# Kernel tuning notes

Measured on AMD Instinct MI355X. Metric: run time of the kernel, lower is better.

Reference implementation:

```python
import jax, jax.numpy as jnp
import numpy as np

DIM, B, H, W = 96, 2, 64, 64
D_INNER, D_STATE, DT_RANK, K = 2 * DIM, 16, 6, 4


def _conv2d(x, w, b=None, padding=0, dilation=1, groups=1):
    out = jax.lax.conv_general_dilated(
        x, w, (1, 1), [(padding, padding)] * 2,
        rhs_dilation=(dilation, dilation),
        dimension_numbers=('NCHW', 'OIHW', 'NCHW'),
        feature_group_count=groups)
    return out if b is None else out + b[None, :, None, None]


def _layernorm(x, g, b, eps=1e-5):
    mu = x.mean(-1, keepdims=True)
    xc = x - mu
    var = (xc * xc).mean(-1, keepdims=True)
    return xc * jax.lax.rsqrt(var + eps) * g + b


def _chan_recal(t, w1, w2):
    s = t.mean((2, 3)) + t.max(axis=(2, 3))          # GAP + GMP, (B,C)
    w = jax.nn.sigmoid(jax.nn.relu(s @ w1.T) @ w2.T)
    return t * w[:, :, None, None]


def _selective_scan(u, delta, A, Bm, Cm, D):
    # u, delta: (B,K,d,L); A: (K,d,N); Bm,Cm: (B,K,N,L); D: (K,d)
    Bsz, Kk, d, L = u.shape
    N = A.shape[-1]
    seq = (jnp.moveaxis(delta, -1, 0), jnp.moveaxis(u, -1, 0),
           jnp.moveaxis(Bm, -1, 0), jnp.moveaxis(Cm, -1, 0))
    h0 = jnp.zeros((Bsz, Kk, d, N), u.dtype)

    def step(h, inp):
        dl, ul, bl, cl = inp  # (B,K,d),(B,K,d),(B,K,N),(B,K,N)
        h = jnp.exp(dl[..., None] * A) * h + (dl * ul)[..., None] * bl[:, :, None, :]
        return h, (h * cl[:, :, None, :]).sum(-1)

    _, ys = jax.lax.scan(step, h0, seq)
    return jnp.moveaxis(ys, 0, -1) + D[None, :, :, None] * u  # (B,K,d,L)


def _ss2d(x, in_proj_w, conv_w, conv_b, x_proj_w, dt_w, dt_b,
          A_logs, Ds, out_norm_g, out_norm_b, out_proj_w):
    Bsz, Hh, Ww, C = x.shape
    d = in_proj_w.shape[0] // 2
    xm, z = jnp.split(x @ in_proj_w.T, 2, axis=-1)
    xm = jnp.transpose(xm, (0, 3, 1, 2))  # (B,d,H,W)
    xm = jax.nn.silu(_conv2d(xm, conv_w, conv_b, padding=1, groups=d))
    L = Hh * Ww
    x_hw = xm.reshape(Bsz, d, L)
    x_wh = jnp.transpose(xm, (0, 1, 3, 2)).reshape(Bsz, d, L)
    xs = jnp.stack([x_hw, x_wh, x_hw[..., ::-1], x_wh[..., ::-1]], axis=1)  # (B,4,d,L)
    x_dbl = jnp.einsum('bkdl,kcd->bkcl', xs, x_proj_w)
    r = dt_w.shape[-1]
    N = A_logs.shape[-1]
    dts, Bs, Cs = jnp.split(x_dbl, [r, r + N], axis=2)
    dts = jax.nn.softplus(jnp.einsum('bkrl,kdr->bkdl', dts, dt_w) + dt_b[None, :, :, None])
    out_y = _selective_scan(xs, dts, -jnp.exp(A_logs), Bs, Cs, Ds)
    inv_y = out_y[:, 2:4, :, ::-1]
    wh = lambda t: jnp.transpose(t.reshape(Bsz, d, Ww, Hh), (0, 1, 3, 2)).reshape(Bsz, d, L)
    y = out_y[:, 0] + inv_y[:, 0] + wh(out_y[:, 1]) + wh(inv_y[:, 1])
    y = _layernorm(jnp.transpose(y, (0, 2, 1)).reshape(Bsz, Hh, Ww, d), out_norm_g, out_norm_b)
    return (y * jax.nn.silu(z)) @ out_proj_w.T


def _forward(x, arf_w1, arf_b1, arf_w2, arf_b2, arf_w3, arf_b3, arf_w4, arf_b4,
             fuse_w, fuse_b, edge_w, enh_w1, enh_b1, bn_g, bn_b, enh_w2, enh_b2,
             pre_fc1, pre_fc2, norm_g, norm_b, in_proj_w, ss_conv_w, ss_conv_b,
             x_proj_w, dt_w, dt_b, A_logs, Ds, out_norm_g, out_norm_b, out_proj_w,
             post_fc1, post_fc2, proj_w, proj_b):
    shortcut = x
    C = x.shape[1]
    g = C // 4
    # AdaptiveReceptiveField (fc gating branch is dead code in the original forward)
    f1 = _conv2d(x, arf_w1, arf_b1, padding=1, dilation=1, groups=g)
    f2 = _conv2d(x, arf_w2, arf_b2, padding=2, dilation=2, groups=g)
    f3 = _conv2d(x, arf_w3, arf_b3, padding=4, dilation=4, groups=g)
    f4 = _conv2d(x, arf_w4, arf_b4, padding=8, dilation=8, groups=g)
    h = _conv2d(jnp.concatenate([f1, f2, f3, f4], 1), fuse_w, fuse_b)
    # LearnableEdgeEnhancement (BatchNorm in training mode: batch stats, biased var)
    edge = _conv2d(h, edge_w, None, padding=1, groups=C)
    e = _conv2d(edge, enh_w1, enh_b1)
    mu = e.mean((0, 2, 3), keepdims=True)
    var = ((e - mu) ** 2).mean((0, 2, 3), keepdims=True)
    e = jax.nn.relu((e - mu) * jax.lax.rsqrt(var + 1e-5) * bn_g[None, :, None, None]
                    + bn_b[None, :, None, None])
    h = h * (1.0 + jax.nn.sigmoid(_conv2d(e, enh_w2, enh_b2)))
    h = _chan_recal(h, pre_fc1, pre_fc2)
    hn = _layernorm(jnp.transpose(h, (0, 2, 3, 1)), norm_g, norm_b)
    hn = _ss2d(hn, in_proj_w, ss_conv_w, ss_conv_b, x_proj_w, dt_w, dt_b,
               A_logs, Ds, out_norm_g, out_norm_b, out_proj_w)
    h = jnp.transpose(hn, (0, 3, 1, 2))
    h = _chan_recal(h, post_fc1, post_fc2)
    h = _conv2d(h, proj_w, proj_b)
    return shortcut + h


def setup_inputs():
    key = jax.random.key(0)
    ks = iter(jax.random.split(key, 48))
    rn = lambda shape, s=0.05: jax.random.normal(next(ks), shape, jnp.float32) * s
    lap = jnp.array([[0., 1., 0.], [1., -4., 1.], [0., 1., 0.]], jnp.float32)
    q = DIM // 4
    inp = {
        'x': jax.random.normal(next(ks), (B, DIM, H, W), jnp.float32),
        'arf_w1': rn((q, 4, 3, 3)), 'arf_b1': rn((q,)),
        'arf_w2': rn((q, 4, 3, 3)), 'arf_b2': rn((q,)),
        'arf_w3': rn((q, 4, 3, 3)), 'arf_b3': rn((q,)),
        'arf_w4': rn((q, 4, 3, 3)), 'arf_b4': rn((q,)),
        'fuse_w': rn((DIM, DIM, 1, 1)), 'fuse_b': rn((DIM,)),
        'edge_w': jnp.tile(lap[None, None], (DIM, 1, 1, 1)),
        'enh_w1': rn((q, DIM, 1, 1)), 'enh_b1': rn((q,)),
        'bn_g': jnp.ones((q,), jnp.float32), 'bn_b': jnp.zeros((q,), jnp.float32),
        'enh_w2': rn((DIM, q, 1, 1)), 'enh_b2': rn((DIM,)),
        'pre_fc1': rn((q, DIM)), 'pre_fc2': rn((DIM, q)),
        'norm_g': jnp.ones((DIM,), jnp.float32), 'norm_b': jnp.zeros((DIM,), jnp.float32),
        'in_proj_w': rn((2 * D_INNER, DIM)),
        'ss_conv_w': rn((D_INNER, 1, 3, 3)), 'ss_conv_b': rn((D_INNER,)),
        'x_proj_w': rn((K, DT_RANK + 2 * D_STATE, D_INNER)),
        'dt_w': rn((K, D_INNER, DT_RANK), 0.1), 'dt_b': rn((K, D_INNER), 0.1),
        'A_logs': jnp.broadcast_to(jnp.log(jnp.arange(1, D_STATE + 1, dtype=jnp.float32)),
                                   (K, D_INNER, D_STATE)) + jnp.zeros((K, D_INNER, D_STATE), jnp.float32),
        'Ds': jnp.ones((K, D_INNER), jnp.float32),
        'out_norm_g': jnp.ones((D_INNER,), jnp.float32),
        'out_norm_b': jnp.zeros((D_INNER,), jnp.float32),
        'out_proj_w': rn((DIM, D_INNER)),
        'post_fc1': rn((q, DIM)), 'post_fc2': rn((DIM, q)),
        'proj_w': rn((DIM, DIM, 1, 1)), 'proj_b': rn((DIM,)),
    }
    return inp


def reference(x, arf_w1, arf_b1, arf_w2, arf_b2, arf_w3, arf_b3, arf_w4, arf_b4,
              fuse_w, fuse_b, edge_w, enh_w1, enh_b1, bn_g, bn_b, enh_w2, enh_b2,
              pre_fc1, pre_fc2, norm_g, norm_b, in_proj_w, ss_conv_w, ss_conv_b,
              x_proj_w, dt_w, dt_b, A_logs, Ds, out_norm_g, out_norm_b, out_proj_w,
              post_fc1, post_fc2, proj_w, proj_b):
    return _forward(x, arf_w1, arf_b1, arf_w2, arf_b2, arf_w3, arf_b3, arf_w4, arf_b4,
                    fuse_w, fuse_b, edge_w, enh_w1, enh_b1, bn_g, bn_b, enh_w2, enh_b2,
                    pre_fc1, pre_fc2, norm_g, norm_b, in_proj_w, ss_conv_w, ss_conv_b,
                    x_proj_w, dt_w, dt_b, A_logs, Ds, out_norm_g, out_norm_b, out_proj_w,
                    post_fc1, post_fc2, proj_w, proj_b)
```

## Files before the change

### kernel.cpp

```cpp
#include <hip/hip_runtime.h>
#include <cmath>

#define LL   4096
#define HWD  64
#define CCH  96
#define QQ   24
#define DDI  192
#define NST  16
#define NCH  128
#define CLEN 32
#define TSC  32
#define XT2  32
#define XP   108
#define FP   100
#define VP   204

static const size_t OFF_F    = 0;
static const size_t OFF_H    = 786432;
static const size_t OFF_E    = 1572864;
static const size_t OFF_E1PS = 1769472;
static const size_t OFF_E1P2 = 1770240;
static const size_t OFF_XM   = 2556736;
static const size_t OFF_Z    = 4129600;
static const size_t OFF_XC   = 5702464;
static const size_t OFF_DTS  = 7275328;
static const size_t OFF_BC   = 13566784;
static const size_t OFF_YK   = 14615360;
static const size_t OFF_Y2   = 22528832;
static const size_t OFF_HL   = 23315264;
static const size_t OFF_SD   = 26460992;
static const size_t OFF_HIN  = 26657600;
static const size_t OFF_S1PS = 29803328;
static const size_t OFF_S1PM = 29806400;
static const size_t OFF_S2PS = 29809472;
static const size_t OFF_S2PM = 29821760;

static __device__ __forceinline__ int map_k(int k, int l) {
  int ll = (k & 2) ? (LL - 1 - l) : l;
  return (k & 1) ? (((ll & 63) << 6) | (ll >> 6)) : ll;
}

__global__ __launch_bounds__(256) void k_arf(const float* __restrict__ x,
    const float* __restrict__ w1, const float* __restrict__ b1,
    const float* __restrict__ w2, const float* __restrict__ b2,
    const float* __restrict__ w3, const float* __restrict__ b3,
    const float* __restrict__ w4, const float* __restrict__ b4,
    float* __restrict__ f) {
  int idx = blockIdx.x * 256 + threadIdx.x;
  int p = idx & (LL - 1);
  int oc = __builtin_amdgcn_readfirstlane((idx >> 12) % CCH);
  int b  = __builtin_amdgcn_readfirstlane(idx / (CCH * LL));
  int i = oc / QQ, q = oc % QQ;
  int dil = 1 << i;
  const float* w  = (i == 0 ? w1 : i == 1 ? w2 : i == 2 ? w3 : w4) + q * 36;
  const float* bb = (i == 0 ? b1 : i == 1 ? b2 : i == 2 ? b3 : b4);
  int yy0 = p >> 6, xx0 = p & 63;
  float acc = bb[q];
  const float* xin = x + ((size_t)b * CCH + q * 4) * LL;
  #pragma unroll
  for (int ky = 0; ky < 3; ky++) {
    int yy = yy0 + (ky - 1) * dil;
    if (yy < 0 || yy >= HWD) continue;
    #pragma unroll
    for (int kx = 0; kx < 3; kx++) {
      int xx = xx0 + (kx - 1) * dil;
      if (xx < 0 || xx >= HWD) continue;
      int pp = (yy << 6) + xx;
      #pragma unroll
      for (int ci = 0; ci < 4; ci++)
        acc += w[ci * 9 + ky * 3 + kx] * xin[(size_t)ci * LL + pp];
    }
  }
  f[idx] = acc;
}

__global__ __launch_bounds__(256) void k_fuse(const float* __restrict__ f,
    const float* __restrict__ fw, const float* __restrict__ fb, float* __restrict__ h) {
  int pix0 = blockIdx.x * 64;
  int oc0 = blockIdx.y * 48;
  int b = pix0 >> 12, p0 = pix0 & (LL - 1);
  int t = threadIdx.x;
  __shared__ float fs[64][FP];
  __shared__ float wbuf[48 * 96];
  for (int i = t; i < 96 * 16; i += 256) {
    int c = i >> 4, q = i & 15;
    float4 v = *(const float4*)(f + ((size_t)b * CCH + c) * LL + p0 + q * 4);
    fs[q * 4 + 0][c] = v.x; fs[q * 4 + 1][c] = v.y;
    fs[q * 4 + 2][c] = v.z; fs[q * 4 + 3][c] = v.w;
  }
  {
    const float4* src = (const float4*)(fw + (size_t)oc0 * CCH);
    float4* dst = (float4*)wbuf;
    for (int i = t; i < 48 * 24; i += 256) dst[i] = src[i];
  }
  __syncthreads();
  int px = t & 63;
  int cg2 = __builtin_amdgcn_readfirstlane(t >> 6);
  float acc[12];
  #pragma unroll
  for (int j = 0; j < 12; j++) acc[j] = 0.f;
  for (int c4 = 0; c4 < 24; c4++) {
    float4 xv = *(const float4*)(&fs[px][c4 * 4]);
    #pragma unroll
    for (int j = 0; j < 12; j++) {
      float4 wv = *(const float4*)(&wbuf[(cg2 * 12 + j) * 96 + c4 * 4]);
      acc[j] = fmaf(xv.x, wv.x, fmaf(xv.y, wv.y, fmaf(xv.z, wv.z, fmaf(xv.w, wv.w, acc[j]))));
    }
  }
  __syncthreads();
  float* ot = &fs[0][0];
  #pragma unroll
  for (int j = 0; j < 12; j++) ot[px * 49 + cg2 * 12 + j] = acc[j];
  __syncthreads();
  for (int i = t; i < 48 * 64; i += 256) {
    int o = i >> 6, p2 = i & 63;
    h[((size_t)b * CCH + oc0 + o) * LL + p0 + p2] = ot[p2 * 49 + o] + fb[oc0 + o];
  }
}

__global__ __launch_bounds__(256) void k_edge(const float* __restrict__ h,
    const float* __restrict__ ew, float* __restrict__ edge) {
  int idx = blockIdx.x * 256 + threadIdx.x;
  int p = idx & (LL - 1);
  int c = __builtin_amdgcn_readfirstlane((idx >> 12) % CCH);
  int b = __builtin_amdgcn_readfirstlane(idx / (CCH * LL));
  int yy0 = p >> 6, xx0 = p & 63;
  const float* w = ew + c * 9;
  const float* hr = h + ((size_t)b * CCH + c) * LL;
  float acc = 0.f;
  #pragma unroll
  for (int ky = 0; ky < 3; ky++) {
    int yy = yy0 + ky - 1;
    if (yy < 0 || yy >= HWD) continue;
    #pragma unroll
    for (int kx = 0; kx < 3; kx++) {
      int xx = xx0 + kx - 1;
      if (xx < 0 || xx >= HWD) continue;
      acc += w[ky * 3 + kx] * hr[(yy << 6) + xx];
    }
  }
  edge[idx] = acc;
}

__global__ __launch_bounds__(256) void k_e1(const float* __restrict__ edge,
    const float* __restrict__ w, const float* __restrict__ bias, float* __restrict__ e,
    float* __restrict__ e1ps, float* __restrict__ e1p2) {
  int tid = threadIdx.x;
  int idx = blockIdx.x * 256 + tid;
  int p = idx & (LL - 1);
  int q = __builtin_amdgcn_readfirstlane((idx >> 12) % QQ);
  int b = __builtin_amdgcn_readfirstlane(idx / (QQ * LL));
  const float* er = edge + (size_t)b * CCH * LL + p;
  const float* wr = w + q * CCH;
  float acc = bias[q];
  for (int c = 0; c < CCH; c++) acc += wr[c] * er[(size_t)c * LL];
  e[idx] = acc;
  __shared__ float rs[256], r2[256];
  rs[tid] = acc; r2[tid] = acc * acc; __syncthreads();
  for (int st = 128; st > 0; st >>= 1) {
    if (tid < st) { rs[tid] += rs[tid + st]; r2[tid] += r2[tid + st]; }
    __syncthreads();
  }
  if (tid == 0) { e1ps[blockIdx.x] = rs[0]; e1p2[blockIdx.x] = r2[0]; }
}

__global__ __launch_bounds__(256) void k_enh(const float* __restrict__ e,
    const float* __restrict__ e1ps, const float* __restrict__ e1p2,
    const float* __restrict__ bn_g, const float* __restrict__ bn_b,
    const float* __restrict__ w2, const float* __restrict__ b2,
    float* __restrict__ h, float* __restrict__ s1ps, float* __restrict__ s1pm) {
  int tid = threadIdx.x;
  __shared__ float bns[QQ], bnsh[QQ];
  if (tid < QQ) {
    float s = 0.f, s2 = 0.f;
    #pragma unroll
    for (int b2 = 0; b2 < 2; b2++)
      for (int i = 0; i < 16; i++) {
        int pi = (b2 * QQ + tid) * 16 + i;
        s += e1ps[pi]; s2 += e1p2[pi];
      }
    float mu = s / (2.f * LL);
    float var = s2 / (2.f * LL) - mu * mu;
    float sc = bn_g[tid] * rsqrtf(var + 1e-5f);
    bns[tid] = sc;
    bnsh[tid] = bn_b[tid] - mu * sc;
  }
  __syncthreads();
  int idx = blockIdx.x * 256 + tid;
  int p = idx & (LL - 1);
  int o = __builtin_amdgcn_readfirstlane((idx >> 12) % CCH);
  int b = __builtin_amdgcn_readfirstlane(idx / (CCH * LL));
  const float* er = e + (size_t)b * QQ * LL + p;
  const float* wr = w2 + o * QQ;
  float acc = b2[o];
  #pragma unroll
  for (int q = 0; q < QQ; q++) {
    float en = fmaxf(er[(size_t)q * LL] * bns[q] + bnsh[q], 0.f);
    acc += wr[q] * en;
  }
  float sig = 1.f / (1.f + __expf(-acc));
  float val = h[idx] * (1.f + sig);
  h[idx] = val;
  __shared__ float rsum[256], rmax[256];
  rsum[tid] = val; rmax[tid] = val; __syncthreads();
  for (int st = 128; st > 0; st >>= 1) {
    if (tid < st) { rsum[tid] += rsum[tid + st]; rmax[tid] = fmaxf(rmax[tid], rmax[tid + st]); }
    __syncthreads();
  }
  if (tid == 0) {
    int row = blockIdx.x >> 4, blk = blockIdx.x & 15;
    s1ps[row * 16 + blk] = rsum[0];
    s1pm[row * 16 + blk] = rmax[0];
  }
}

__global__ __launch_bounds__(256) void k_inproj(const float* __restrict__ h,
    const float* __restrict__ s1ps, const float* __restrict__ s1pm,
    const float* __restrict__ fc1, const float* __restrict__ fc2,
    const float* __restrict__ ng, const float* __restrict__ nb,
    const float* __restrict__ W, float* __restrict__ xm, float* __restrict__ z) {
  int pix0 = blockIdx.x * 64;
  int oc0 = blockIdx.y * CCH;
  int b = pix0 >> 12, p0 = pix0 & (LL - 1);
  int t = threadIdx.x;
  __shared__ float xs[64][XP];
  __shared__ float wbuf[CCH * CCH];
  __shared__ float wsm[CCH];
  __shared__ float hid[QQ];
  __shared__ float ps[64][4], ps2[64][4];
  __shared__ float mu_s[64], rs_s[64];
  if (t < CCH) {
    const float4* sp = (const float4*)(s1ps + (size_t)(b * CCH + t) * 16);
    const float4* mp = (const float4*)(s1pm + (size_t)(b * CCH + t) * 16);
    float s = 0.f, m = -3.402823466e38f;
    #pragma unroll
    for (int i = 0; i < 4; i++) {
      float4 a = sp[i]; s += a.x + a.y + a.z + a.w;
      float4 c = mp[i]; m = fmaxf(m, fmaxf(fmaxf(c.x, c.y), fmaxf(c.z, c.w)));
    }
    wsm[t] = s / (float)LL + m;
  }
  __syncthreads();
  if (t < QQ) {
    float a = 0.f;
    for (int c = 0; c < CCH; c++) a += wsm[c] * fc1[t * CCH + c];
    hid[t] = fmaxf(a, 0.f);
  }
  __syncthreads();
  float w1v = 0.f;
  if (t < CCH) {
    float a = 0.f;
    #pragma unroll
    for (int q = 0; q < QQ; q++) a += hid[q] * fc2[t * QQ + q];
    w1v = 1.f / (1.f + __expf(-a));
  }
  __syncthreads();
  if (t < CCH) wsm[t] = w1v;
  {
    const float4* src = (const float4*)(W + (size_t)oc0 * CCH);
    float4* dst = (float4*)wbuf;
    for (int i = t; i < CCH * 24; i += 256) dst[i] = src[i];
  }
  __syncthreads();
  for (int i = t; i < CCH * 16; i += 256) {
    int c = i >> 4, q = i & 15;
    float w = wsm[c];
    float4 v = *(const float4*)(h + ((size_t)b * CCH + c) * LL + p0 + q * 4);
    xs[q * 4 + 0][c] = v.x * w; xs[q * 4 + 1][c] = v.y * w;
    xs[q * 4 + 2][c] = v.z * w; xs[q * 4 + 3][c] = v.w * w;
  }
  __syncthreads();
  {
    int px = t & 63, qr = t >> 6;
    float s = 0.f, s2 = 0.f;
    #pragma unroll
    for (int j = 0; j < 24; j++) { float v = xs[px][qr * 24 + j]; s += v; s2 += v * v; }
    ps[px][qr] = s; ps2[px][qr] = s2;
  }
  __syncthreads();
  if (t < 64) {
    float ss = ps[t][0] + ps[t][1] + ps[t][2] + ps[t][3];
    float ss2 = ps2[t][0] + ps2[t][1] + ps2[t][2] + ps2[t][3];
    float mu = ss / (float)CCH;
    mu_s[t] = mu;
    rs_s[t] = rsqrtf(ss2 / (float)CCH - mu * mu + 1e-5f);
  }
  __syncthreads();
  for (int i = t; i < 64 * CCH; i += 256) {
    int px = i / CCH, c = i % CCH;
    xs[px][c] = (xs[px][c] - mu_s[px]) * rs_s[px] * ng[c] + nb[c];
  }
  __syncthreads();
  int li = t & 63;
  int cg2 = __builtin_amdgcn_readfirstlane(t >> 6);
  float acc[24];
  #pragma unroll
  for (int j = 0; j < 24; j++) acc[j] = 0.f;
  for (int dq = 0; dq < 24; dq++) {
    float4 xv = *(const float4*)(&xs[li][dq * 4]);
    #pragma unroll
    for (int j = 0; j < 24; j++) {
      float4 wv = *(const float4*)(&wbuf[(cg2 + 4 * j) * CCH + dq * 4]);
      acc[j] = fmaf(xv.x, wv.x, fmaf(xv.y, wv.y, fmaf(xv.z, wv.z, fmaf(xv.w, wv.w, acc[j]))));
    }
  }
  __syncthreads();
  float* ot = &xs[0][0];
  #pragma unroll
  for (int j = 0; j < 24; j++) ot[li * 97 + cg2 + 4 * j] = acc[j];
  __syncthreads();
  float* dst = (oc0 < DDI) ? xm : z;
  int od0 = oc0 % DDI;
  for (int i = t; i < 64 * 96; i += 256) {
    int row = i / 96, c = i % 96;
    dst[(size_t)(pix0 + row) * DDI + od0 + c] = ot[row * 97 + c];
  }
}

__global__ __launch_bounds__(256) void k_ssconv(const float* __restrict__ xm,
    const float* __restrict__ w, const float* __restrict__ bias, float* __restrict__ xc) {
  int idx = blockIdx.x * 256 + threadIdx.x;
  int d = idx % DDI;
  int rem = idx / DDI;
  int xx0 = rem & 63;
  int y0 = ((rem >> 6) & 31) * 2;
  int b = idx / (DDI * LL / 2);
  float wv[9];
  #pragma unroll
  for (int i = 0; i < 9; i++) wv[i] = w[d * 9 + i];
  float acc0 = bias[d], acc1 = bias[d];
  const float* xr = xm + (size_t)b * LL * DDI + d;
  #pragma unroll
  for (int ky = -1; ky <= 2; ky++) {
    int yy = y0 + ky;
    if (yy < 0 || yy >= HWD) continue;
    #pragma unroll
    for (int kx = -1; kx <= 1; kx++) {
      int xx = xx0 + kx;
      if (xx < 0 || xx >= HWD) continue;
      float val = xr[(size_t)((yy << 6) + xx) * DDI];
      if (ky <= 1) acc0 += wv[(ky + 1) * 3 + (kx + 1)] * val;
      if (ky >= 0) acc1 += wv[ky * 3 + (kx + 1)] * val;
    }
  }
  size_t o0 = ((size_t)b * LL + (y0 << 6) + xx0) * DDI + d;
  xc[o0] = acc0 / (1.f + __expf(-acc0));
  xc[o0 + 64 * DDI] = acc1 / (1.f + __expf(-acc1));
}

__global__ __launch_bounds__(256) void k_xdbl(const float* __restrict__ xc,
    const float* __restrict__ xpw, float* __restrict__ dtr_ws, float* __restrict__ bcb) {
  int lt = blockIdx.x;
  int bk = blockIdx.y;
  int b = bk >> 2, k = bk & 3;
  int t = threadIdx.x;
  __shared__ float xs[XT2][XP];
  __shared__ float wbuf[38 * 96];
  int l0 = lt * XT2;
  int pos = t & 31;
  int cg2 = t >> 5;
  float acc[5];
  #pragma unroll
  for (int j = 0; j < 5; j++) acc[j] = 0.f;
  for (int h = 0; h < 2; h++) {
    __syncthreads();
    for (int i = t; i < XT2 * 24; i += 256) {
      int row = i / 24, dq = i % 24;
      int p = map_k(k, l0 + row);
      *(float4*)(&xs[row][dq * 4]) =
          *(const float4*)(xc + ((size_t)b * LL + p) * DDI + h * 96 + dq * 4);
    }
    for (int i = t; i < 38 * 24; i += 256) {
      int c = i / 24, dq = i % 24;
      *(float4*)(&wbuf[c * 96 + dq * 4]) =
          *(const float4*)(xpw + ((size_t)k * 38 + c) * DDI + h * 96 + dq * 4);
    }
    __syncthreads();
    for (int dq = 0; dq < 24; dq++) {
      float4 xv = *(const float4*)(&xs[pos][dq * 4]);
      #pragma unroll
      for (int j = 0; j < 5; j++) {
        int c = cg2 + 8 * j;
        if (c < 38) {
          float4 wv = *(const float4*)(&wbuf[c * 96 + dq * 4]);
          acc[j] = fmaf(xv.x, wv.x, fmaf(xv.y, wv.y, fmaf(xv.z, wv.z, fmaf(xv.w, wv.w, acc[j]))));
        }
      }
    }
  }
  #pragma unroll
  for (int j = 0; j < 5; j++) {
    int c = cg2 + 8 * j;
    if (c < 6) dtr_ws[((size_t)bk * LL + l0 + pos) * 6 + c] = acc[j];
    else if (c < 38) bcb[((size_t)bk * LL + l0 + pos) * 32 + (c - 6)] = acc[j];
  }
}

template <int PASS>
__global__ __launch_bounds__(192) void k_scan(const float* __restrict__ dtr_ws,
    const float* __restrict__ bcb, const float* __restrict__ xc,
    const float* __restrict__ A_logs, const float* __restrict__ dtw,
    const float* __restrict__ dtb, float* __restrict__ hl, float* __restrict__ sd,
    const float* __restrict__ hin, float* __restrict__ yk) {
  int ch = blockIdx.x, bk = blockIdx.y;
  int b = bk >> 2, k = bk & 3;
  int d = threadIdx.x;
  __shared__ float u_s[TSC][DDI];
  __shared__ float bcs[TSC][32];
  __shared__ float dtr_s[TSC][6];
  float Av[NST];
  #pragma unroll
  for (int n = 0; n < NST; n++) Av[n] = -__expf(A_logs[(size_t)(k * DDI + d) * NST + n]);
  bool pw = true;
  #pragma unroll
  for (int n = 1; n < NST; n++) pw = pw && (fabsf(Av[n] - (float)(n + 1) * Av[0]) <= 1e-3f * (n + 1));
  float wdt[6];
  #pragma unroll
  for (int r = 0; r < 6; r++) wdt[r] = dtw[((size_t)(k * DDI + d)) * 6 + r];
  float bdt = dtb[k * DDI + d];
  float h[NST];
  if (PASS == 0) {
    #pragma unroll
    for (int n = 0; n < NST; n++) h[n] = 0.f;
  } else {
    const float* hp = hin + ((size_t)(bk * DDI + d) * NCH + ch) * NST;
    #pragma unroll
    for (int n = 0; n < NST; n++) h[n] = hp[n];
  }
  float sumdt = 0.f;
  int l0 = ch * CLEN;
  {
    for (int i = d; i < TSC * (DDI / 4); i += 192) {
      int row = i / (DDI / 4), q = i % (DDI / 4);
      int p = map_k(k, l0 + row);
      ((float4*)u_s)[i] = *(const float4*)(xc + ((size_t)b * LL + p) * DDI + q * 4);
    }
    {
      const float4* src = (const float4*)(bcb + ((size_t)bk * LL + l0) * 32);
      float4* dst = (float4*)bcs;
      for (int i = d; i < TSC * 32 / 4; i += 192) dst[i] = src[i];
    }
    for (int i = d; i < TSC * 6; i += 192)
      ((float*)dtr_s)[i] = dtr_ws[((size_t)bk * LL + l0) * 6 + i];
    __syncthreads();
    for (int tt = 0; tt < TSC; tt++) {
      float a = bdt;
      #pragma unroll
      for (int r = 0; r < 6; r++) a = fmaf(wdt[r], dtr_s[tt][r], a);
      float dt = (a > 15.f) ? a : __logf(1.f + __expf(a));
      float u  = u_s[tt][d];
      float dtu = dt * u;
      if (PASS == 0) sumdt += dt;
      float eA[NST];
      if (pw) {
        float E = __expf(dt * Av[0]);
        float en = 1.f;
        #pragma unroll
        for (int n = 0; n < NST; n++) { en *= E; eA[n] = en; }
      } else {
        #pragma unroll
        for (int n = 0; n < NST; n++) eA[n] = __expf(dt * Av[n]);
      }
      float y = 0.f;
      #pragma unroll
      for (int n = 0; n < NST; n++) {
        h[n] = eA[n] * h[n] + dtu * bcs[tt][n];
        y += h[n] * bcs[tt][16 + n];
      }
      if (PASS == 1) {
        int p = map_k(k, l0 + tt);
        yk[((size_t)bk * LL + p) * DDI + d] = y;
      }
    }
  }
  if (PASS == 0) {
    float* hp = hl + ((size_t)(bk * DDI + d) * NCH + ch) * NST;
    #pragma unroll
    for (int n = 0; n < NST; n++) hp[n] = h[n];
    sd[(size_t)(bk * DDI + d) * NCH + ch] = sumdt;
  }
}

__global__ __launch_bounds__(256) void k_carry(const float* __restrict__ A_logs,
    const float* __restrict__ hl, const float* __restrict__ sd, float* __restrict__ hin) {
  int idx = blockIdx.x * 256 + threadIdx.x;
  int n = idx & 15;
  int d = (idx >> 4) % DDI;
  int bk = idx / (DDI * NST);
  int k = bk & 3;
  float Aval = -__expf(A_logs[(size_t)(k * DDI + d) * NST + n]);
  float h = 0.f;
  size_t base = (size_t)(bk * DDI + d) * NCH;
  for (int ch = 0; ch < NCH; ch++) {
    hin[(base + ch) * NST + n] = h;
    h = __expf(Aval * sd[base + ch]) * h + hl[(base + ch) * NST + n];
  }
}

__global__ __launch_bounds__(256) void k_outproj(const float* __restrict__ yk,
    const float* __restrict__ xc, const float* __restrict__ Ds, const float* __restrict__ z,
    const float* __restrict__ ong, const float* __restrict__ onb,
    const float* __restrict__ W, float* __restrict__ y2,
    float* __restrict__ s2ps, float* __restrict__ s2pm) {
  int pix0 = blockIdx.x * 64;
  int oc0 = blockIdx.y * 48;
  int b = pix0 >> 12, p0 = pix0 & (LL - 1);
  int t = threadIdx.x;
  __shared__ float xs[64][VP];
  __shared__ float wbuf[48 * 96];
  __shared__ float dsum[DDI];
  __shared__ float ps[64][4], ps2[64][4];
  __shared__ float mu_s[64], rs_s[64];
  if (t < 48) {
    float4 a  = *(const float4*)(Ds + t * 4);
    float4 c1 = *(const float4*)(Ds + DDI + t * 4);
    float4 c2 = *(const float4*)(Ds + 2 * DDI + t * 4);
    float4 c3 = *(const float4*)(Ds + 3 * DDI + t * 4);
    *(float4*)(&dsum[t * 4]) = make_float4(a.x + c1.x + c2.x + c3.x, a.y + c1.y + c2.y + c3.y,
                                           a.z + c1.z + c2.z + c3.z, a.w + c1.w + c2.w + c3.w);
  }
  __syncthreads();
  int px = t & 63, qr = t >> 6;
  int p = p0 + px;
  size_t pb = ((size_t)b * LL + p) * DDI;
  size_t yb = ((size_t)b * 4 * LL + p) * DDI;
  {
    float s = 0.f, s2 = 0.f;
    #pragma unroll
    for (int j = 0; j < 12; j++) {
      int c = (qr * 12 + j) * 4;
      float4 y0 = *(const float4*)(yk + yb + c);
      float4 y1 = *(const float4*)(yk + yb + (size_t)LL * DDI + c);
      float4 y2v = *(const float4*)(yk + yb + 2ul * LL * DDI + c);
      float4 y3 = *(const float4*)(yk + yb + 3ul * LL * DDI + c);
      float4 u = *(const float4*)(xc + pb + c);
      float4 dv = *(const float4*)(&dsum[c]);
      float4 v;
      v.x = y0.x + y1.x + y2v.x + y3.x + dv.x * u.x;
      v.y = y0.y + y1.y + y2v.y + y3.y + dv.y * u.y;
      v.z = y0.z + y1.z + y2v.z + y3.z + dv.z * u.z;
      v.w = y0.w + y1.w + y2v.w + y3.w + dv.w * u.w;
      *(float4*)(&xs[px][c]) = v;
      s += v.x + v.y + v.z + v.w;
      s2 += v.x * v.x + v.y * v.y + v.z * v.z + v.w * v.w;
    }
    ps[px][qr] = s; ps2[px][qr] = s2;
  }
  __syncthreads();
  if (t < 64) {
    float ss = ps[t][0] + ps[t][1] + ps[t][2] + ps[t][3];
    float ss2 = ps2[t][0] + ps2[t][1] + ps2[t][2] + ps2[t][3];
    float mu = ss / (float)DDI;
    mu_s[t] = mu;
    rs_s[t] = rsqrtf(ss2 / (float)DDI - mu * mu + 1e-5f);
  }
  __syncthreads();
  {
    float mu = mu_s[px], rs = rs_s[px];
    #pragma unroll
    for (int j = 0; j < 12; j++) {
      int c = (qr * 12 + j) * 4;
      float4 v = *(const float4*)(&xs[px][c]);
      float4 zz = *(const float4*)(z + pb + c);
      float4 og = *(const float4*)(ong + c);
      float4 ob = *(const float4*)(onb + c);
      float4 gv;
      gv.x = ((v.x - mu) * rs * og.x + ob.x) * (zz.x / (1.f + __expf(-zz.x)));
      gv.y = ((v.y - mu) * rs * og.y + ob.y) * (zz.y / (1.f + __expf(-zz.y)));
      gv.z = ((v.z - mu) * rs * og.z + ob.z) * (zz.z / (1.f + __expf(-zz.z)));
      gv.w = ((v.w - mu) * rs * og.w + ob.w) * (zz.w / (1.f + __expf(-zz.w)));
      *(float4*)(&xs[px][c]) = gv;
    }
  }
  int li = px;
  int cg2 = __builtin_amdgcn_readfirstlane(qr);
  float acc[12];
  #pragma unroll
  for (int j = 0; j < 12; j++) acc[j] = 0.f;
  for (int hh = 0; hh < 2; hh++) {
    __syncthreads();
    for (int i = t; i < 48 * 24; i += 256) {
      int c = i / 24, dq = i % 24;
      *(float4*)(&wbuf[c * 96 + dq * 4]) =
          *(const float4*)(W + (size_t)(oc0 + c) * DDI + hh * 96 + dq * 4);
    }
    __syncthreads();
    for (int dq = 0; dq < 24; dq++) {
      float4 xv = *(const float4*)(&xs[li][hh * 96 + dq * 4]);
      #pragma unroll
      for (int j = 0; j < 12; j++) {
        float4 wv = *(const float4*)(&wbuf[(cg2 + 4 * j) * 96 + dq * 4]);
        acc[j] = fmaf(xv.x, wv.x, fmaf(xv.y, wv.y, fmaf(xv.z, wv.z, fmaf(xv.w, wv.w, acc[j]))));
      }
    }
  }
  int lane = t & 63;
  #pragma unroll
  for (int j = 0; j < 12; j++) {
    float sv = acc[j], mv = acc[j];
    #pragma unroll
    for (int o = 32; o > 0; o >>= 1) {
      sv += __shfl_xor(sv, o);
      mv = fmaxf(mv, __shfl_xor(mv, o));
    }
    if (lane == 0) {
      int oc = oc0 + cg2 + 4 * j;
      int tile = blockIdx.x & 63;
      s2ps[(size_t)(b * CCH + oc) * 64 + tile] = sv;
      s2pm[(size_t)(b * CCH + oc) * 64 + tile] = mv;
    }
  }
  __syncthreads();
  float* ot = &xs[0][0];
  #pragma unroll
  for (int j = 0; j < 12; j++) ot[li * 49 + cg2 + 4 * j] = acc[j];
  __syncthreads();
  for (int i = t; i < 48 * 64; i += 256) {
    int o = i / 64, pi = i % 64;
    y2[((size_t)b * CCH + oc0 + o) * LL + p0 + pi] = ot[pi * 49 + o];
  }
}

__global__ __launch_bounds__(256) void k_final(const float* __restrict__ x,
    const float* __restrict__ y2, const float* __restrict__ s2ps, const float* __restrict__ s2pm,
    const float* __restrict__ fc1, const float* __restrict__ fc2,
    const float* __restrict__ pw, const float* __restrict__ pb, float* __restrict__ out) {
  int pix0 = blockIdx.x * 64;
  int oc0 = blockIdx.y * 48;
  int b = pix0 >> 12, p0 = pix0 & (LL - 1);
  int t = threadIdx.x;
  __shared__ float fs[64][FP];
  __shared__ float wbuf[48 * 96];
  __shared__ float wsm[CCH];
  __shared__ float hid[QQ];
  if (t < CCH) {
    const float4* sp = (const float4*)(s2ps + (size_t)(b * CCH + t) * 64);
    const float4* mp = (const float4*)(s2pm + (size_t)(b * CCH + t) * 64);
    float s = 0.f, m = -3.402823466e38f;
    #pragma unroll
    for (int i = 0; i < 16; i++) {
      float4 a = sp[i]; s += a.x + a.y + a.z + a.w;
      float4 c = mp[i]; m = fmaxf(m, fmaxf(fmaxf(c.x, c.y), fmaxf(c.z, c.w)));
    }
    wsm[t] = s / (float)LL + m;
  }
  __syncthreads();
  if (t < QQ) {
    float a = 0.f;
    for (int c = 0; c < CCH; c++) a += wsm[c] * fc1[t * CCH + c];
    hid[t] = fmaxf(a, 0.f);
  }
  __syncthreads();
  float w2v = 0.f;
  if (t < CCH) {
    float a = 0.f;
    #pragma unroll
    for (int q = 0; q < QQ; q++) a += hid[q] * fc2[t * QQ + q];
    w2v = 1.f / (1.f + __expf(-a));
  }
  __syncthreads();
  if (t < CCH) wsm[t] = w2v;
  __syncthreads();
  for (int i = t; i < 96 * 16; i += 256) {
    int c = i >> 4, q = i & 15;
    float4 v = *(const float4*)(y2 + ((size_t)b * CCH + c) * LL + p0 + q * 4);
    fs[q * 4 + 0][c] = v.x; fs[q * 4 + 1][c] = v.y;
    fs[q * 4 + 2][c] = v.z; fs[q * 4 + 3][c] = v.w;
  }
  for (int i = t; i < 48 * 24; i += 256) {
    int row = i / 24, q = i % 24;
    float4 wv = *(const float4*)(pw + (size_t)(oc0 + row) * CCH + q * 4);
    ((float4*)wbuf)[i] = make_float4(wv.x * wsm[q * 4], wv.y * wsm[q * 4 + 1],
                                     wv.z * wsm[q * 4 + 2], wv.w * wsm[q * 4 + 3]);
  }
  __syncthreads();
  int px = t & 63;
  int cg2 = __builtin_amdgcn_readfirstlane(t >> 6);
  float acc[12];
  #pragma unroll
  for (int j = 0; j < 12; j++) acc[j] = 0.f;
  for (int c4 = 0; c4 < 24; c4++) {
    float4 xv = *(const float4*)(&fs[px][c4 * 4]);
    #pragma unroll
    for (int j = 0; j < 12; j++) {
      float4 wv = *(const float4*)(&wbuf[(cg2 * 12 + j) * 96 + c4 * 4]);
      acc[j] = fmaf(xv.x, wv.x, fmaf(xv.y, wv.y, fmaf(xv.z, wv.z, fmaf(xv.w, wv.w, acc[j]))));
    }
  }
  __syncthreads();
  float* ot = &fs[0][0];
  #pragma unroll
  for (int j = 0; j < 12; j++) ot[px * 49 + cg2 * 12 + j] = acc[j];
  __syncthreads();
  for (int i = t; i < 48 * 64; i += 256) {
    int o = i >> 6, p2 = i & 63;
    size_t oi = ((size_t)b * CCH + oc0 + o) * LL + p0 + p2;
    out[oi] = x[oi] + pb[oc0 + o] + ot[p2 * 49 + o];
  }
}

extern "C" void kernel_launch(void* const* d_in, const int* in_sizes, int n_in,
                              void* d_out, int out_size, void* d_ws, size_t ws_size,
                              hipStream_t stream) {
  const float* x        = (const float*)d_in[0];
  const float* arf_w1   = (const float*)d_in[1];
  const float* arf_b1   = (const float*)d_in[2];
  const float* arf_w2   = (const float*)d_in[3];
  const float* arf_b2   = (const float*)d_in[4];
  const float* arf_w3   = (const float*)d_in[5];
  const float* arf_b3   = (const float*)d_in[6];
  const float* arf_w4   = (const float*)d_in[7];
  const float* arf_b4   = (const float*)d_in[8];
  const float* fuse_w   = (const float*)d_in[9];
  const float* fuse_b   = (const float*)d_in[10];
  const float* edge_w   = (const float*)d_in[11];
  const float* enh_w1   = (const float*)d_in[12];
  const float* enh_b1   = (const float*)d_in[13];
  const float* bn_g     = (const float*)d_in[14];
  const float* bn_b     = (const float*)d_in[15];
  const float* enh_w2   = (const float*)d_in[16];
  const float* enh_b2   = (const float*)d_in[17];
  const float* pre_fc1  = (const float*)d_in[18];
  const float* pre_fc2  = (const float*)d_in[19];
  const float* norm_g   = (const float*)d_in[20];
  const float* norm_b   = (const float*)d_in[21];
  const float* in_proj_w= (const float*)d_in[22];
  const float* ss_conv_w= (const float*)d_in[23];
  const float* ss_conv_b= (const float*)d_in[24];
  const float* x_proj_w = (const float*)d_in[25];
  const float* dt_w     = (const float*)d_in[26];
  const float* dt_b     = (const float*)d_in[27];
  const float* A_logs   = (const float*)d_in[28];
  const float* Ds       = (const float*)d_in[29];
  const float* out_ng   = (const float*)d_in[30];
  const float* out_nb   = (const float*)d_in[31];
  const float* out_proj_w = (const float*)d_in[32];
  const float* post_fc1 = (const float*)d_in[33];
  const float* post_fc2 = (const float*)d_in[34];
  const float* proj_w   = (const float*)d_in[35];
  const float* proj_b   = (const float*)d_in[36];

  float* ws = (float*)d_ws;
  float* fbuf  = ws + OFF_F;
  float* hbuf  = ws + OFF_H;
  float* ebuf  = ws + OFF_E;
  float* e1ps  = ws + OFF_E1PS;
  float* e1p2  = ws + OFF_E1P2;
  float* xmbuf = ws + OFF_XM;
  float* zbuf  = ws + OFF_Z;
  float* xcbuf = ws + OFF_XC;
  float* dtrbuf= ws + OFF_DTS;
  float* bcbuf = ws + OFF_BC;
  float* ykbuf = ws + OFF_YK;
  float* y2buf = ws + OFF_Y2;
  float* hlbuf = ws + OFF_HL;
  float* sdbuf = ws + OFF_SD;
  float* hinbuf= ws + OFF_HIN;
  float* s1ps  = ws + OFF_S1PS;
  float* s1pm  = ws + OFF_S1PM;
  float* s2ps  = ws + OFF_S2PS;
  float* s2pm  = ws + OFF_S2PM;

  k_arf<<<3072, 256, 0, stream>>>(x, arf_w1, arf_b1, arf_w2, arf_b2, arf_w3, arf_b3, arf_w4, arf_b4, fbuf);
  k_fuse<<<dim3(128, 2), 256, 0, stream>>>(fbuf, fuse_w, fuse_b, hbuf);
  k_edge<<<3072, 256, 0, stream>>>(hbuf, edge_w, fbuf);
  k_e1<<<768, 256, 0, stream>>>(fbuf, enh_w1, enh_b1, ebuf, e1ps, e1p2);
  k_enh<<<3072, 256, 0, stream>>>(ebuf, e1ps, e1p2, bn_g, bn_b, enh_w2, enh_b2, hbuf, s1ps, s1pm);
  k_inproj<<<dim3(128, 4), 256, 0, stream>>>(hbuf, s1ps, s1pm, pre_fc1, pre_fc2, norm_g, norm_b, in_proj_w, xmbuf, zbuf);
  k_ssconv<<<3072, 256, 0, stream>>>(xmbuf, ss_conv_w, ss_conv_b, xcbuf);
  k_xdbl<<<dim3(LL / XT2, 8), 256, 0, stream>>>(xcbuf, x_proj_w, dtrbuf, bcbuf);
  k_scan<0><<<dim3(NCH, 8), 192, 0, stream>>>(dtrbuf, bcbuf, xcbuf, A_logs, dt_w, dt_b, hlbuf, sdbuf, nullptr, nullptr);
  k_carry<<<96, 256, 0, stream>>>(A_logs, hlbuf, sdbuf, hinbuf);
  k_scan<1><<<dim3(NCH, 8), 192, 0, stream>>>(dtrbuf, bcbuf, xcbuf, A_logs, dt_w, dt_b, nullptr, nullptr, hinbuf, ykbuf);
  k_outproj<<<dim3(128, 2), 256, 0, stream>>>(ykbuf, xcbuf, Ds, zbuf, out_ng, out_nb, out_proj_w, y2buf, s2ps, s2pm);
  k_final<<<dim3(128, 2), 256, 0, stream>>>(x, y2buf, s2ps, s2pm, post_fc1, post_fc2, proj_w, proj_b, (float*)d_out);
  (void)in_sizes; (void)n_in; (void)out_size; (void)ws_size;
}
```

Baseline: 221.6 us.

## Fuse edge conv with enh 1x1 conv, and x_proj with scan pass 0

The depthwise edge conv and the first 1x1 enhancement conv now run in one row-tiled kernel. It keeps the edge output in shared memory and reduces BN partial sums with wave shuffles, with the partial-sum layout widened to 64 per channel. The x_proj projection is fused with the first chunked-scan pass, so dt/B/C are consumed straight from shared memory and xc is loaded once per chunk. This cuts two launches and a global round trip of the edge tensor and xc. The edge kernel now has only 128 blocks with large shared memory, which may underfill the GPU.

Result: slower. 256.1 us (+15.5%).

```diff
diff --git a/kernel.cpp b/kernel.cpp
--- a/kernel.cpp
+++ b/kernel.cpp
@@ -19,7 +19,7 @@
 static const size_t OFF_H    = 786432;
 static const size_t OFF_E    = 1572864;
 static const size_t OFF_E1PS = 1769472;
-static const size_t OFF_E1P2 = 1770240;
+static const size_t OFF_E1P2 = 1772544;
 static const size_t OFF_XM   = 2556736;
 static const size_t OFF_Z    = 4129600;
 static const size_t OFF_XC   = 5702464;
@@ -118,50 +118,66 @@
   }
 }
 
-__global__ __launch_bounds__(256) void k_edge(const float* __restrict__ h,
-    const float* __restrict__ ew, float* __restrict__ edge) {
-  int idx = blockIdx.x * 256 + threadIdx.x;
-  int p = idx & (LL - 1);
-  int c = __builtin_amdgcn_readfirstlane((idx >> 12) % CCH);
-  int b = __builtin_amdgcn_readfirstlane(idx / (CCH * LL));
-  int yy0 = p >> 6, xx0 = p & 63;
-  const float* w = ew + c * 9;
-  const float* hr = h + ((size_t)b * CCH + c) * LL;
-  float acc = 0.f;
-  #pragma unroll
-  for (int ky = 0; ky < 3; ky++) {
-    int yy = yy0 + ky - 1;
-    if (yy < 0 || yy >= HWD) continue;
-    #pragma unroll
-    for (int kx = 0; kx < 3; kx++) {
-      int xx = xx0 + kx - 1;
-      if (xx < 0 || xx >= HWD) continue;
-      acc += w[ky * 3 + kx] * hr[(yy << 6) + xx];
-    }
-  }
-  edge[idx] = acc;
-}
-
-__global__ __launch_bounds__(256) void k_e1(const float* __restrict__ edge,
-    const float* __restrict__ w, const float* __restrict__ bias, float* __restrict__ e,
-    float* __restrict__ e1ps, float* __restrict__ e1p2) {
-  int tid = threadIdx.x;
-  int idx = blockIdx.x * 256 + tid;
-  int p = idx & (LL - 1);
-  int q = __builtin_amdgcn_readfirstlane((idx >> 12) % QQ);
-  int b = __builtin_amdgcn_readfirstlane(idx / (QQ * LL));
-  const float* er = edge + (size_t)b * CCH * LL + p;
-  const float* wr = w + q * CCH;
-  float acc = bias[q];
-  for (int c = 0; c < CCH; c++) acc += wr[c] * er[(size_t)c * LL];
-  e[idx] = acc;
-  __shared__ float rs[256], r2[256];
-  rs[tid] = acc; r2[tid] = acc * acc; __syncthreads();
-  for (int st = 128; st > 0; st >>= 1) {
-    if (tid < st) { rs[tid] += rs[tid + st]; r2[tid] += r2[tid + st]; }
-    __syncthreads();
-  }
-  if (tid == 0) { e1ps[blockIdx.x] = rs[0]; e1p2[blockIdx.x] = r2[0]; }
+__global__ __launch_bounds__(256) void k_edge1(const float* __restrict__ h,
+    const float* __restrict__ ew, const float* __restrict__ w1, const float* __restrict__ bias,
+    float* __restrict__ e, float* __restrict__ e1ps, float* __restrict__ e1p2) {
+  int blk = blockIdx.x;
+  int b = blk >> 6, y = blk & 63;
+  int t = threadIdx.x;
+  __shared__ float hs[96][3][64];
+  __shared__ float el[64][XP];
+  __shared__ float wbuf[QQ * CCH];
+  for (int i = t; i < 96 * 3 * 16; i += 256) {
+    int c = i / 48, rem = i % 48, r = rem / 16, q = rem % 16;
+    int yy = y + r - 1;
+    float4 v = make_float4(0.f, 0.f, 0.f, 0.f);
+    if (yy >= 0 && yy < HWD)
+      v = *(const float4*)(h + ((size_t)b * CCH + c) * LL + (yy << 6) + q * 4);
+    *(float4*)(&hs[c][r][q * 4]) = v;
+  }
+  for (int i = t; i < QQ * 24; i += 256) ((float4*)wbuf)[i] = ((const float4*)w1)[i];
+  __syncthreads();
+  int px = t & 63, wg = t >> 6;
+  for (int j = 0; j < 24; j++) {
+    int c = wg * 24 + j;
+    const float* wc = ew + c * 9;
+    float acc = 0.f;
+    #pragma unroll
+    for (int r = 0; r < 3; r++) {
+      #pragma unroll
+      for (int dx = -1; dx <= 1; dx++) {
+        int xx = px + dx;
+        if (xx >= 0 && xx < 64) acc += wc[r * 3 + (dx + 1)] * hs[c][r][xx];
+      }
+    }
+    el[px][c] = acc;
+  }
+  __syncthreads();
+  float accq[6];
+  #pragma unroll
+  for (int jj = 0; jj < 6; jj++) accq[jj] = bias[wg * 6 + jj];
+  for (int c4 = 0; c4 < 24; c4++) {
+    float4 xv = *(const float4*)(&el[px][c4 * 4]);
+    #pragma unroll
+    for (int jj = 0; jj < 6; jj++) {
+      float4 wv = *(const float4*)(&wbuf[(wg * 6 + jj) * CCH + c4 * 4]);
+      accq[jj] = fmaf(xv.x, wv.x, fmaf(xv.y, wv.y, fmaf(xv.z, wv.z, fmaf(xv.w, wv.w, accq[jj]))));
+    }
+  }
+  #pragma unroll
+  for (int jj = 0; jj < 6; jj++)
+    e[((size_t)b * QQ + wg * 6 + jj) * LL + (y << 6) + px] = accq[jj];
+  #pragma unroll
+  for (int jj = 0; jj < 6; jj++) {
+    float s = accq[jj], s2 = accq[jj] * accq[jj];
+    #pragma unroll
+    for (int o = 32; o > 0; o >>= 1) { s += __shfl_xor(s, o); s2 += __shfl_xor(s2, o); }
+    if (px == 0) {
+      int q = wg * 6 + jj;
+      e1ps[((size_t)b * QQ + q) * 64 + y] = s;
+      e1p2[((size_t)b * QQ + q) * 64 + y] = s2;
+    }
+  }
 }
 
 __global__ __launch_bounds__(256) void k_enh(const float* __restrict__ e,
@@ -175,8 +191,8 @@
     float s = 0.f, s2 = 0.f;
     #pragma unroll
     for (int b2 = 0; b2 < 2; b2++)
-      for (int i = 0; i < 16; i++) {
-        int pi = (b2 * QQ + tid) * 16 + i;
+      for (int i = 0; i < 64; i++) {
+        int pi = (b2 * QQ + tid) * 64 + i;
         s += e1ps[pi]; s2 += e1p2[pi];
       }
     float mu = s / (2.f * LL);
@@ -348,36 +364,39 @@
   xc[o0 + 64 * DDI] = acc1 / (1.f + __expf(-acc1));
 }
 
-__global__ __launch_bounds__(256) void k_xdbl(const float* __restrict__ xc,
-    const float* __restrict__ xpw, float* __restrict__ dtr_ws, float* __restrict__ bcb) {
+__global__ __launch_bounds__(256) void k_xscan0(const float* __restrict__ xc,
+    const float* __restrict__ xpw, const float* __restrict__ A_logs,
+    const float* __restrict__ dtw, const float* __restrict__ dtb,
+    float* __restrict__ dtr_ws, float* __restrict__ bcb,
+    float* __restrict__ hl, float* __restrict__ sd) {
   int lt = blockIdx.x;
   int bk = blockIdx.y;
   int b = bk >> 2, k = bk & 3;
   int t = threadIdx.x;
-  __shared__ float xs[XT2][XP];
+  __shared__ float xs[XT2][VP];
   __shared__ float wbuf[38 * 96];
+  __shared__ float dtr_s[XT2][6];
+  __shared__ float bcs[XT2][32];
   int l0 = lt * XT2;
-  int pos = t & 31;
-  int cg2 = t >> 5;
+  for (int i = t; i < XT2 * 48; i += 256) {
+    int row = i / 48, dq = i % 48;
+    int p = map_k(k, l0 + row);
+    *(float4*)(&xs[row][dq * 4]) = *(const float4*)(xc + ((size_t)b * LL + p) * DDI + dq * 4);
+  }
+  int pos = t & 31, cg2 = t >> 5;
   float acc[5];
   #pragma unroll
   for (int j = 0; j < 5; j++) acc[j] = 0.f;
-  for (int h = 0; h < 2; h++) {
+  for (int hh = 0; hh < 2; hh++) {
     __syncthreads();
-    for (int i = t; i < XT2 * 24; i += 256) {
-      int row = i / 24, dq = i % 24;
-      int p = map_k(k, l0 + row);
-      *(float4*)(&xs[row][dq * 4]) =
-          *(const float4*)(xc + ((size_t)b * LL + p) * DDI + h * 96 + dq * 4);
-    }
     for (int i = t; i < 38 * 24; i += 256) {
       int c = i / 24, dq = i % 24;
       *(float4*)(&wbuf[c * 96 + dq * 4]) =
-          *(const float4*)(xpw + ((size_t)k * 38 + c) * DDI + h * 96 + dq * 4);
+          *(const float4*)(xpw + ((size_t)k * 38 + c) * DDI + hh * 96 + dq * 4);
     }
     __syncthreads();
     for (int dq = 0; dq < 24; dq++) {
-      float4 xv = *(const float4*)(&xs[pos][dq * 4]);
+      float4 xv = *(const float4*)(&xs[pos][hh * 96 + dq * 4]);
       #pragma unroll
       for (int j = 0; j < 5; j++) {
         int c = cg2 + 8 * j;
@@ -391,66 +410,38 @@
   #pragma unroll
   for (int j = 0; j < 5; j++) {
     int c = cg2 + 8 * j;
-    if (c < 6) dtr_ws[((size_t)bk * LL + l0 + pos) * 6 + c] = acc[j];
-    else if (c < 38) bcb[((size_t)bk * LL + l0 + pos) * 32 + (c - 6)] = acc[j];
-  }
-}
-
-template <int PASS>
-__global__ __launch_bounds__(192) void k_scan(const float* __restrict__ dtr_ws,
-    const float* __restrict__ bcb, const float* __restrict__ xc,
-    const float* __restrict__ A_logs, const float* __restrict__ dtw,
-    const float* __restrict__ dtb, float* __restrict__ hl, float* __restrict__ sd,
-    const float* __restrict__ hin, float* __restrict__ yk) {
-  int ch = blockIdx.x, bk = blockIdx.y;
-  int b = bk >> 2, k = bk & 3;
-  int d = threadIdx.x;
-  __shared__ float u_s[TSC][DDI];
-  __shared__ float bcs[TSC][32];
-  __shared__ float dtr_s[TSC][6];
-  float Av[NST];
-  #pragma unroll
-  for (int n = 0; n < NST; n++) Av[n] = -__expf(A_logs[(size_t)(k * DDI + d) * NST + n]);
-  bool pw = true;
-  #pragma unroll
-  for (int n = 1; n < NST; n++) pw = pw && (fabsf(Av[n] - (float)(n + 1) * Av[0]) <= 1e-3f * (n + 1));
-  float wdt[6];
-  #pragma unroll
-  for (int r = 0; r < 6; r++) wdt[r] = dtw[((size_t)(k * DDI + d)) * 6 + r];
-  float bdt = dtb[k * DDI + d];
-  float h[NST];
-  if (PASS == 0) {
-    #pragma unroll
-    for (int n = 0; n < NST; n++) h[n] = 0.f;
-  } else {
-    const float* hp = hin + ((size_t)(bk * DDI + d) * NCH + ch) * NST;
-    #pragma unroll
-    for (int n = 0; n < NST; n++) h[n] = hp[n];
-  }
-  float sumdt = 0.f;
-  int l0 = ch * CLEN;
-  {
-    for (int i = d; i < TSC * (DDI / 4); i += 192) {
-      int row = i / (DDI / 4), q = i % (DDI / 4);
-      int p = map_k(k, l0 + row);
-      ((float4*)u_s)[i] = *(const float4*)(xc + ((size_t)b * LL + p) * DDI + q * 4);
-    }
-    {
-      const float4* src = (const float4*)(bcb + ((size_t)bk * LL + l0) * 32);
-      float4* dst = (float4*)bcs;
-      for (int i = d; i < TSC * 32 / 4; i += 192) dst[i] = src[i];
-    }
-    for (int i = d; i < TSC * 6; i += 192)
-      ((float*)dtr_s)[i] = dtr_ws[((size_t)bk * LL + l0) * 6 + i];
-    __syncthreads();
+    if (c < 6) {
+      dtr_s[pos][c] = acc[j];
+      dtr_ws[((size_t)bk * LL + l0 + pos) * 6 + c] = acc[j];
+    } else if (c < 38) {
+      bcs[pos][c - 6] = acc[j];
+      bcb[((size_t)bk * LL + l0 + pos) * 32 + (c - 6)] = acc[j];
+    }
+  }
+  __syncthreads();
+  int d = t;
+  if (d < DDI) {
+    float Av[NST];
+    #pragma unroll
+    for (int n = 0; n < NST; n++) Av[n] = -__expf(A_logs[(size_t)(k * DDI + d) * NST + n]);
+    bool pw = true;
+    #pragma unroll
+    for (int n = 1; n < NST; n++) pw = pw && (fabsf(Av[n] - (float)(n + 1) * Av[0]) <= 1e-3f * (n + 1));
+    float wdt[6];
+    #pragma unroll
+    for (int r = 0; r < 6; r++) wdt[r] = dtw[((size_t)(k * DDI + d)) * 6 + r];
+    float bdt = dtb[k * DDI + d];
+    float hst[NST];
+    #pragma unroll
+    for (int n = 0; n < NST; n++) hst[n] = 0.f;
+    float sumdt = 0.f;
     for (int tt = 0; tt < TSC; tt++) {
       float a = bdt;
       #pragma unroll
       for (int r = 0; r < 6; r++) a = fmaf(wdt[r], dtr_s[tt][r], a);
       float dt = (a > 15.f) ? a : __logf(1.f + __expf(a));
-      float u  = u_s[tt][d];
-      float dtu = dt * u;
-      if (PASS == 0) sumdt += dt;
+      float dtu = dt * xs[tt][d];
+      sumdt += dt;
       float eA[NST];
       if (pw) {
         float E = __expf(dt * Av[0]);
@@ -461,23 +452,80 @@
         #pragma unroll
         for (int n = 0; n < NST; n++) eA[n] = __expf(dt * Av[n]);
       }
-      float y = 0.f;
       #pragma unroll
-      for (int n = 0; n < NST; n++) {
-        h[n] = eA[n] * h[n] + dtu * bcs[tt][n];
-        y += h[n] * bcs[tt][16 + n];
-      }
-      if (PASS == 1) {
-        int p = map_k(k, l0 + tt);
-        yk[((size_t)bk * LL + p) * DDI + d] = y;
-      }
-    }
-  }
-  if (PASS == 0) {
-    float* hp = hl + ((size_t)(bk * DDI + d) * NCH + ch) * NST;
-    #pragma unroll
-    for (int n = 0; n < NST; n++) hp[n] = h[n];
-    sd[(size_t)(bk * DDI + d) * NCH + ch] = sumdt;
+      for (int n = 0; n < NST; n++) hst[n] = eA[n] * hst[n] + dtu * bcs[tt][n];
+    }
+    float* hp = hl + ((size_t)(bk * DDI + d) * NCH + lt) * NST;
+    #pragma unroll
+    for (int n = 0; n < NST; n++) hp[n] = hst[n];
+    sd[(size_t)(bk * DDI + d) * NCH + lt] = sumdt;
+  }
+}
+
+__global__ __launch_bounds__(192) void k_scan1(const float* __restrict__ dtr_ws,
+    const float* __restrict__ bcb, const float* __restrict__ xc,
+    const float* __restrict__ A_logs, const float* __restrict__ dtw,
+    const float* __restrict__ dtb, const float* __restrict__ hin, float* __restrict__ yk) {
+  int ch = blockIdx.x, bk = blockIdx.y;
+  int b = bk >> 2, k = bk & 3;
+  int d = threadIdx.x;
+  __shared__ float u_s[TSC][DDI];
+  __shared__ float bcs[TSC][32];
+  __shared__ float dtr_s[TSC][6];
+  float Av[NST];
+  #pragma unroll
+  for (int n = 0; n < NST; n++) Av[n] = -__expf(A_logs[(size_t)(k * DDI + d) * NST + n]);
+  bool pw = true;
+  #pragma unroll
+  for (int n = 1; n < NST; n++) pw = pw && (fabsf(Av[n] - (float)(n + 1) * Av[0]) <= 1e-3f * (n + 1));
+  float wdt[6];
+  #pragma unroll
+  for (int r = 0; r < 6; r++) wdt[r] = dtw[((size_t)(k * DDI + d)) * 6 + r];
+  float bdt = dtb[k * DDI + d];
+  float h[NST];
+  {
+    const float* hp = hin + ((size_t)(bk * DDI + d) * NCH + ch) * NST;
+    #pragma unroll
+    for (int n = 0; n < NST; n++) h[n] = hp[n];
+  }
+  int l0 = ch * CLEN;
+  for (int i = d; i < TSC * (DDI / 4); i += 192) {
+    int row = i / (DDI / 4), q = i % (DDI / 4);
+    int p = map_k(k, l0 + row);
+    ((float4*)u_s)[i] = *(const float4*)(xc + ((size_t)b * LL + p) * DDI + q * 4);
+  }
+  {
+    const float4* src = (const float4*)(bcb + ((size_t)bk * LL + l0) * 32);
+    float4* dst = (float4*)bcs;
+    for (int i = d; i < TSC * 32 / 4; i += 192) dst[i] = src[i];
+  }
+  for (int i = d; i < TSC * 6; i += 192)
+    ((float*)dtr_s)[i] = dtr_ws[((size_t)bk * LL + l0) * 6 + i];
+  __syncthreads();
+  for (int tt = 0; tt < TSC; tt++) {
+    float a = bdt;
+    #pragma unroll
+    for (int r = 0; r < 6; r++) a = fmaf(wdt[r], dtr_s[tt][r], a);
+    float dt = (a > 15.f) ? a : __logf(1.f + __expf(a));
+    float dtu = dt * u_s[tt][d];
+    float eA[NST];
+    if (pw) {
+      float E = __expf(dt * Av[0]);
+      float en = 1.f;
+      #pragma unroll
+      for (int n = 0; n < NST; n++) { en *= E; eA[n] = en; }
+    } else {
+      #pragma unroll
+      for (int n = 0; n < NST; n++) eA[n] = __expf(dt * Av[n]);
+    }
+    float y = 0.f;
+    #pragma unroll
+    for (int n = 0; n < NST; n++) {
+      h[n] = eA[n] * h[n] + dtu * bcs[tt][n];
+      y += h[n] * bcs[tt][16 + n];
+    }
+    int p = map_k(k, l0 + tt);
+    yk[((size_t)bk * LL + p) * DDI + d] = y;
   }
 }
 
@@ -763,15 +811,13 @@
 
   k_arf<<<3072, 256, 0, stream>>>(x, arf_w1, arf_b1, arf_w2, arf_b2, arf_w3, arf_b3, arf_w4, arf_b4, fbuf);
   k_fuse<<<dim3(128, 2), 256, 0, stream>>>(fbuf, fuse_w, fuse_b, hbuf);
-  k_edge<<<3072, 256, 0, stream>>>(hbuf, edge_w, fbuf);
-  k_e1<<<768, 256, 0, stream>>>(fbuf, enh_w1, enh_b1, ebuf, e1ps, e1p2);
+  k_edge1<<<128, 256, 0, stream>>>(hbuf, edge_w, enh_w1, enh_b1, ebuf, e1ps, e1p2);
   k_enh<<<3072, 256, 0, stream>>>(ebuf, e1ps, e1p2, bn_g, bn_b, enh_w2, enh_b2, hbuf, s1ps, s1pm);
   k_inproj<<<dim3(128, 4), 256, 0, stream>>>(hbuf, s1ps, s1pm, pre_fc1, pre_fc2, norm_g, norm_b, in_proj_w, xmbuf, zbuf);
   k_ssconv<<<3072, 256, 0, stream>>>(xmbuf, ss_conv_w, ss_conv_b, xcbuf);
-  k_xdbl<<<dim3(LL / XT2, 8), 256, 0, stream>>>(xcbuf, x_proj_w, dtrbuf, bcbuf);
-  k_scan<0><<<dim3(NCH, 8), 192, 0, stream>>>(dtrbuf, bcbuf, xcbuf, A_logs, dt_w, dt_b, hlbuf, sdbuf, nullptr, nullptr);
+  k_xscan0<<<dim3(NCH, 8), 256, 0, stream>>>(xcbuf, x_proj_w, A_logs, dt_w, dt_b, dtrbuf, bcbuf, hlbuf, sdbuf);
   k_carry<<<96, 256, 0, stream>>>(A_logs, hlbuf, sdbuf, hinbuf);
-  k_scan<1><<<dim3(NCH, 8), 192, 0, stream>>>(dtrbuf, bcbuf, xcbuf, A_logs, dt_w, dt_b, nullptr, nullptr, hinbuf, ykbuf);
+  k_scan1<<<dim3(NCH, 8), 192, 0, stream>>>(dtrbuf, bcbuf, xcbuf, A_logs, dt_w, dt_b, hinbuf, ykbuf);
   k_outproj<<<dim3(128, 2), 256, 0, stream>>>(ykbuf, xcbuf, Ds, zbuf, out_ng, out_nb, out_proj_w, y2buf, s2ps, s2pm);
   k_final<<<dim3(128, 2), 256, 0, stream>>>(x, y2buf, s2ps, s2pm, post_fc1, post_fc2, proj_w, proj_b, (float*)d_out);
   (void)in_sizes; (void)n_in; (void)out_size; (void)ws_size;
```
